# Optimization experiments

Measured on AMD Instinct MI355X. Metric: run time of the kernel, lower is better.

## Reference

```python
import jax, jax.numpy as jnp
import numpy as np

B, D, E, H = 4, 128, 512, 512

def setup_inputs() -> dict:
    key = jax.random.key(0)
    k1, k2, k3, k4, k5 = jax.random.split(key, 5)
    s = 1.0 / np.sqrt(H)
    return {
        "x_decoder": jax.random.normal(k1, (B, D, H), dtype=jnp.float32),
        "x_encoder": jax.random.normal(k2, (B, E, H), dtype=jnp.float32),
        "mask": jnp.zeros((B, E), dtype=bool),
        "W1": jax.random.uniform(k3, (H, H), jnp.float32, -s, s),  # nn.Linear weight (out,in)
        "W2": jax.random.uniform(k4, (H, H), jnp.float32, -s, s),
        "v": jax.random.uniform(k5, (H,), jnp.float32, -s, s),     # Linear(H,1) weight squeezed
    }

def reference(x_decoder, x_encoder, mask, W1, W2, v):
    # w1(x_encoder): (B,E,H); w2(x_decoder): (B,D,H)
    enc_t = jnp.einsum('beh,oh->beo', x_encoder, W1)
    dec_t = jnp.einsum('bdh,oh->bdo', x_decoder, W2)
    # additive attention: tanh over broadcast sum (B,D,E,H), reduce with v -> (B,D,E)
    prod = jnp.einsum('bdeh,h->bde', jnp.tanh(dec_t[:, :, None, :] + enc_t[:, None, :, :]), v)
    prod = jnp.where(mask[:, None, :], -jnp.inf, prod)
    return jax.nn.log_softmax(prod, axis=-1)
```

## Files before the change

### kernel.cpp

```cpp
#include <hip/hip_runtime.h>
#include <math.h>

#define BATCH 4
#define DDIM  128
#define EDIM  512
#define HDIM  512

#define TANH_SCALE 2.8853900817779268f

typedef short short8v __attribute__((ext_vector_type(8)));
typedef float f32x4   __attribute__((ext_vector_type(4)));
typedef float f32x2   __attribute__((ext_vector_type(2)));

#define EXP2F(x) __builtin_amdgcn_exp2f(x)
#define RCPF(x)  __builtin_amdgcn_rcpf(x)

static __device__ inline unsigned short f2bf(float f) {
    unsigned u = __float_as_uint(f);
    return (unsigned short)((u + 0x7FFFu + ((u >> 16) & 1u)) >> 16);
}
static __device__ inline unsigned pack_bf2(float f0, float f1) {
    unsigned u0 = __float_as_uint(f0), u1 = __float_as_uint(f1);
    u0 += 0x7FFFu + ((u0 >> 16) & 1u);
    u1 += 0x7FFFu + ((u1 >> 16) & 1u);
    return __builtin_amdgcn_perm(u1, u0, 0x07060302u);
}
static __device__ inline float bf2f(unsigned short h) {
    return __uint_as_float(((unsigned)h) << 16);
}

__global__ __launch_bounds__(256)
void gemm_both(const float* __restrict__ xdec, const float* __restrict__ W2,
               const float* __restrict__ xenc, const float* __restrict__ W1,
               unsigned short* __restrict__ P, unsigned short* __restrict__ Q) {
    __shared__ unsigned short As[2][64][40];
    __shared__ unsigned short Bs[2][64][40];

    const int id = blockIdx.x;
    const float *Ab, *Bb;
    unsigned short* Cb;
    int m0, n0;
    if (id < 64) {
        int b = id >> 4, r = id & 15;
        m0 = (r >> 3) * 64; n0 = (r & 7) * 64;
        Ab = xdec + (long)b * DDIM * HDIM;
        Bb = W2;
        Cb = P + (long)b * DDIM * HDIM;
    } else {
        int t2 = id - 64;
        int b = t2 >> 6, r = t2 & 63;
        m0 = (r >> 3) * 64; n0 = (r & 7) * 64;
        Ab = W1;
        Bb = xenc + (long)b * EDIM * HDIM;
        Cb = Q + (long)b * HDIM * EDIM;
    }

    const int t    = threadIdx.x;
    const int srow = t >> 2;
    const int skq  = (t & 3) << 3;

    const int wid = t >> 6, wm = wid >> 1, wn = wid & 1;
    const int l   = t & 63, lr = l & 15, c16 = l >> 4;

    f32x4 acc[2][2] = {};

    const float* ap = Ab + (long)(m0 + srow) * HDIM + skq;
    const float* bp = Bb + (long)(n0 + srow) * HDIM + skq;

    float4 a0 = *(const float4*)ap, a1 = *(const float4*)(ap + 4);
    float4 b0 = *(const float4*)bp, b1 = *(const float4*)(bp + 4);

    int cur = 0;
    for (int k0 = 0; k0 < HDIM; k0 += 32) {
        uint4 apk, bpk;
        apk.x = pack_bf2(a0.x, a0.y); apk.y = pack_bf2(a0.z, a0.w);
        apk.z = pack_bf2(a1.x, a1.y); apk.w = pack_bf2(a1.z, a1.w);
        bpk.x = pack_bf2(b0.x, b0.y); bpk.y = pack_bf2(b0.z, b0.w);
        bpk.z = pack_bf2(b1.x, b1.y); bpk.w = pack_bf2(b1.z, b1.w);
        *(uint4*)&As[cur][srow][skq] = apk;
        *(uint4*)&Bs[cur][srow][skq] = bpk;

        if (k0 + 32 < HDIM) {
            ap += 32; bp += 32;
            a0 = *(const float4*)ap; a1 = *(const float4*)(ap + 4);
            b0 = *(const float4*)bp; b1 = *(const float4*)(bp + 4);
        }

        asm volatile("s_waitcnt lgkmcnt(0)" ::: "memory");
        __builtin_amdgcn_s_barrier();
        __builtin_amdgcn_sched_barrier(0);

        short8v af[2], bf[2];
        #pragma unroll
        for (int fm = 0; fm < 2; ++fm)
            af[fm] = *(const short8v*)&As[cur][wm * 32 + fm * 16 + lr][c16 * 8];
        #pragma unroll
        for (int fn = 0; fn < 2; ++fn)
            bf[fn] = *(const short8v*)&Bs[cur][wn * 32 + fn * 16 + lr][c16 * 8];
        #pragma unroll
        for (int fm = 0; fm < 2; ++fm)
            #pragma unroll
            for (int fn = 0; fn < 2; ++fn)
                acc[fm][fn] = __builtin_amdgcn_mfma_f32_16x16x32_bf16(
                    af[fm], bf[fn], acc[fm][fn], 0, 0, 0);
        cur ^= 1;
    }

    const int crow = c16 << 2;
    #pragma unroll
    for (int fm = 0; fm < 2; ++fm)
        #pragma unroll
        for (int fn = 0; fn < 2; ++fn)
            #pragma unroll
            for (int r = 0; r < 4; ++r) {
                int rr = m0 + wm * 32 + fm * 16 + crow + r;
                int cc = n0 + wn * 32 + fn * 16 + lr;
                Cb[(long)rr * 512 + cc] = f2bf(EXP2F(TANH_SCALE * acc[fm][fn][r]));
            }
}

__global__ __launch_bounds__(1024)
void attn_lsm(const unsigned short* __restrict__ P,
              const unsigned short* __restrict__ Q,
              const unsigned char* __restrict__ mask,
              const float* __restrict__ vw,
              float* __restrict__ out) {
    const int g    = blockIdx.x;
    const int xcd  = g & 7;
    const int b    = xcd & 3;
    const int dp   = (g >> 3) + ((xcd >> 2) << 5);
    const int pair = b * 64 + dp;
    const int bd0  = pair * 2;
    const int t    = threadIdx.x;
    const int eq   = t & 127;
    const int hg   = t >> 7;

    __shared__ f32x2 combo2[256][3];
    __shared__ float lds[8][128][9];
    __shared__ float red[16];

    if (t < 256) {
        int h = t * 2;
        f32x2 p0, p1, vv;
        p0.x = bf2f(P[bd0 * HDIM + h]);       p0.y = bf2f(P[bd0 * HDIM + h + 1]);
        p1.x = bf2f(P[(bd0 + 1) * HDIM + h]); p1.y = bf2f(P[(bd0 + 1) * HDIM + h + 1]);
        vv.x = -2.0f * vw[h];                 vv.y = -2.0f * vw[h + 1];
        combo2[t][0] = p0; combo2[t][1] = p1; combo2[t][2] = vv;
    }
    __syncthreads();

    const unsigned short* qb = Q + b * HDIM * EDIM + (hg * 64) * EDIM + eq * 4;
    float a00 = 0.f, a01 = 0.f, a02 = 0.f, a03 = 0.f;
    float a10 = 0.f, a11 = 0.f, a12 = 0.f, a13 = 0.f;
    f32x2 ones; ones.x = 1.0f; ones.y = 1.0f;

#define PAIR_SET(Pp, q0p, q1p, VV, accA, accB)                                  \
    {                                                                           \
        f32x2 xp, yp, den, tt, num;                                             \
        asm("v_pk_fma_f32 %0, %1, %2, %3 op_sel_hi:[0,1,1]"                     \
            : "=v"(xp) : "v"(Pp), "v"(q0p), "v"(ones));                         \
        asm("v_pk_fma_f32 %0, %1, %2, %3 op_sel:[1,0,0] op_sel_hi:[1,1,1]"      \
            : "=v"(yp) : "v"(Pp), "v"(q1p), "v"(ones));                         \
        asm("v_pk_mul_f32 %0, %1, %2" : "=v"(den) : "v"(xp), "v"(yp));          \
        asm("v_pk_mul_f32 %0, %1, %2 op_sel:[1,0] op_sel_hi:[1,1]"              \
            : "=v"(tt) : "v"(VV), "v"(xp));                                     \
        asm("v_pk_fma_f32 %0, %1, %2, %3 op_sel_hi:[0,1,1]"                     \
            : "=v"(num) : "v"(VV), "v"(yp), "v"(tt));                           \
        accA = fmaf(num.x, RCPF(den.x), accA);                                  \
        accB = fmaf(num.y, RCPF(den.y), accB);                                  \
    }

    #pragma unroll 4
    for (int ii = 0; ii < 32; ++ii) {
        uint2 qv0 = *(const uint2*)(qb + (size_t)(2 * ii) * EDIM);
        uint2 qv1 = *(const uint2*)(qb + (size_t)(2 * ii + 1) * EDIM);
        f32x2 P0 = combo2[hg * 32 + ii][0];
        f32x2 P1 = combo2[hg * 32 + ii][1];
        f32x2 VV = combo2[hg * 32 + ii][2];
        f32x2 qA0, qB0, qA1, qB1;
        qA0.x = __uint_as_float(qv0.x << 16);
        qA0.y = __uint_as_float(qv0.x & 0xffff0000u);
        qB0.x = __uint_as_float(qv0.y << 16);
        qB0.y = __uint_as_float(qv0.y & 0xffff0000u);
        qA1.x = __uint_as_float(qv1.x << 16);
        qA1.y = __uint_as_float(qv1.x & 0xffff0000u);
        qB1.x = __uint_as_float(qv1.y << 16);
        qB1.y = __uint_as_float(qv1.y & 0xffff0000u);

        PAIR_SET(P0, qA0, qA1, VV, a00, a01);
        PAIR_SET(P0, qB0, qB1, VV, a02, a03);
        PAIR_SET(P1, qA0, qA1, VV, a10, a11);
        PAIR_SET(P1, qB0, qB1, VV, a12, a13);
    }
#undef PAIR_SET

    float* myl = &lds[hg][eq][0];
    myl[0] = a00; myl[1] = a01; myl[2] = a02; myl[3] = a03;
    myl[4] = a10; myl[5] = a11; myl[6] = a12; myl[7] = a13;
    __syncthreads();

    const int d = t >> 9, e = t & 511;
    const int j = d * 4 + (e & 3), eqi = e >> 2;
    float acc = ((lds[0][eqi][j] + lds[1][eqi][j]) +
                 (lds[2][eqi][j] + lds[3][eqi][j])) +
                ((lds[4][eqi][j] + lds[5][eqi][j]) +
                 (lds[6][eqi][j] + lds[7][eqi][j]));

    const bool mk = mask[b * EDIM + e];
    float val = mk ? -INFINITY : acc;

    const int wv = t >> 6, lid = t & 63, dg8 = d * 8;

    float m = val;
    #pragma unroll
    for (int o = 32; o >= 1; o >>= 1) m = fmaxf(m, __shfl_xor(m, o));
    if (lid == 0) red[wv] = m;
    __syncthreads();
    m = red[dg8];
    #pragma unroll
    for (int i = 1; i < 8; ++i) m = fmaxf(m, red[dg8 + i]);
    __syncthreads();

    float s = __expf(val - m);
    #pragma unroll
    for (int o = 32; o >= 1; o >>= 1) s += __shfl_xor(s, o);
    if (lid == 0) red[wv] = s;
    __syncthreads();
    float tot = 0.f;
    #pragma unroll
    for (int i = 0; i < 8; ++i) tot += red[dg8 + i];

    out[(long)(bd0 + d) * EDIM + e] = val - m - __logf(tot);
}

extern "C" void kernel_launch(void* const* d_in, const int* in_sizes, int n_in,
                              void* d_out, int out_size, void* d_ws, size_t ws_size,
                              hipStream_t stream) {
    const float*         xdec = (const float*)d_in[0];
    const float*         xenc = (const float*)d_in[1];
    const unsigned char* mask = (const unsigned char*)d_in[2];
    const float*         W1   = (const float*)d_in[3];
    const float*         W2   = (const float*)d_in[4];
    const float*         vw   = (const float*)d_in[5];
    float*               out  = (float*)d_out;

    unsigned short* P = (unsigned short*)d_ws;
    unsigned short* Q = P + 262144;

    gemm_both<<<320, 256, 0, stream>>>(xdec, W2, xenc, W1, P, Q);
    attn_lsm<<<256, 1024, 0, stream>>>(P, Q, mask, vw, out);
}
```

Measured before the change: 30.61 us.

## Combine four h-terms per reciprocal and widen Q loads to 16 bytes

The attention kernel now merges two pairs of rational tanh terms over a common denominator, so each group of four h values needs one reciprocal per output lane instead of two. Threads are remapped to cover 8 encoder columns and 32 h rows using uint4 loads of Q, with 16 h-groups instead of 8. The cross-thread reduction therefore adds 16 partials from a new LDS layout. It trades reciprocals and load instructions for extra packed multiplies, more LDS traffic, and a wider product of four denominators that risks overflow or precision loss.

```diff
diff --git a/kernel.cpp b/kernel.cpp
--- a/kernel.cpp
+++ b/kernel.cpp
@@ -28,6 +28,8 @@
 static __device__ inline float bf2f(unsigned short h) {
     return __uint_as_float(((unsigned)h) << 16);
 }
+static __device__ inline float blo(unsigned u) { return __uint_as_float(u << 16); }
+static __device__ inline float bhi(unsigned u) { return __uint_as_float(u & 0xffff0000u); }
 
 __global__ __launch_bounds__(256)
 void gemm_both(const float* __restrict__ xdec, const float* __restrict__ W2,
@@ -132,11 +134,11 @@
     const int pair = b * 64 + dp;
     const int bd0  = pair * 2;
     const int t    = threadIdx.x;
-    const int eq   = t & 127;
-    const int hg   = t >> 7;
+    const int eq   = t & 63;
+    const int hg   = t >> 6;
 
     __shared__ f32x2 combo2[256][3];
-    __shared__ float lds[8][128][9];
+    __shared__ float lds_red[16][16][64];
     __shared__ float red[16];
 
     if (t < 256) {
@@ -149,62 +151,97 @@
     }
     __syncthreads();
 
-    const unsigned short* qb = Q + b * HDIM * EDIM + (hg * 64) * EDIM + eq * 4;
-    float a00 = 0.f, a01 = 0.f, a02 = 0.f, a03 = 0.f;
-    float a10 = 0.f, a11 = 0.f, a12 = 0.f, a13 = 0.f;
+    const unsigned short* qb = Q + b * HDIM * EDIM + (hg * 32) * EDIM + eq * 8;
+    f32x2 acc2[2][4] = {};
     f32x2 ones; ones.x = 1.0f; ones.y = 1.0f;
 
-#define PAIR_SET(Pp, q0p, q1p, VV, accA, accB)                                  \
+#define QUAD(P01, P23, VV01, VV23, q0, q1, q2, q3, accp)                        \
     {                                                                           \
-        f32x2 xp, yp, den, tt, num;                                             \
-        asm("v_pk_fma_f32 %0, %1, %2, %3 op_sel_hi:[0,1,1]"                     \
-            : "=v"(xp) : "v"(Pp), "v"(q0p), "v"(ones));                         \
+        f32x2 x0, x1, x2, x3, d1, d2, t1, n1, t2, n2, nn, n, den;               \
+        asm("v_pk_fma_f32 %0, %1, %2, %3 op_sel_hi:[0,1,1]"                     \
+            : "=v"(x0) : "v"(P01), "v"(q0), "v"(ones));                         \
         asm("v_pk_fma_f32 %0, %1, %2, %3 op_sel:[1,0,0] op_sel_hi:[1,1,1]"      \
-            : "=v"(yp) : "v"(Pp), "v"(q1p), "v"(ones));                         \
-        asm("v_pk_mul_f32 %0, %1, %2" : "=v"(den) : "v"(xp), "v"(yp));          \
+            : "=v"(x1) : "v"(P01), "v"(q1), "v"(ones));                         \
+        asm("v_pk_fma_f32 %0, %1, %2, %3 op_sel_hi:[0,1,1]"                     \
+            : "=v"(x2) : "v"(P23), "v"(q2), "v"(ones));                         \
+        asm("v_pk_fma_f32 %0, %1, %2, %3 op_sel:[1,0,0] op_sel_hi:[1,1,1]"      \
+            : "=v"(x3) : "v"(P23), "v"(q3), "v"(ones));                         \
+        asm("v_pk_mul_f32 %0, %1, %2" : "=v"(d1) : "v"(x0), "v"(x1));           \
+        asm("v_pk_mul_f32 %0, %1, %2" : "=v"(d2) : "v"(x2), "v"(x3));           \
         asm("v_pk_mul_f32 %0, %1, %2 op_sel:[1,0] op_sel_hi:[1,1]"              \
-            : "=v"(tt) : "v"(VV), "v"(xp));                                     \
-        asm("v_pk_fma_f32 %0, %1, %2, %3 op_sel_hi:[0,1,1]"                     \
-            : "=v"(num) : "v"(VV), "v"(yp), "v"(tt));                           \
-        accA = fmaf(num.x, RCPF(den.x), accA);                                  \
-        accB = fmaf(num.y, RCPF(den.y), accB);                                  \
-    }
-
-    #pragma unroll 4
-    for (int ii = 0; ii < 32; ++ii) {
-        uint2 qv0 = *(const uint2*)(qb + (size_t)(2 * ii) * EDIM);
-        uint2 qv1 = *(const uint2*)(qb + (size_t)(2 * ii + 1) * EDIM);
-        f32x2 P0 = combo2[hg * 32 + ii][0];
-        f32x2 P1 = combo2[hg * 32 + ii][1];
-        f32x2 VV = combo2[hg * 32 + ii][2];
-        f32x2 qA0, qB0, qA1, qB1;
-        qA0.x = __uint_as_float(qv0.x << 16);
-        qA0.y = __uint_as_float(qv0.x & 0xffff0000u);
-        qB0.x = __uint_as_float(qv0.y << 16);
-        qB0.y = __uint_as_float(qv0.y & 0xffff0000u);
-        qA1.x = __uint_as_float(qv1.x << 16);
-        qA1.y = __uint_as_float(qv1.x & 0xffff0000u);
-        qB1.x = __uint_as_float(qv1.y << 16);
-        qB1.y = __uint_as_float(qv1.y & 0xffff0000u);
-
-        PAIR_SET(P0, qA0, qA1, VV, a00, a01);
-        PAIR_SET(P0, qB0, qB1, VV, a02, a03);
-        PAIR_SET(P1, qA0, qA1, VV, a10, a11);
-        PAIR_SET(P1, qB0, qB1, VV, a12, a13);
-    }
-#undef PAIR_SET
-
-    float* myl = &lds[hg][eq][0];
-    myl[0] = a00; myl[1] = a01; myl[2] = a02; myl[3] = a03;
-    myl[4] = a10; myl[5] = a11; myl[6] = a12; myl[7] = a13;
+            : "=v"(t1) : "v"(VV01), "v"(x0));                                   \
+        asm("v_pk_fma_f32 %0, %1, %2, %3 op_sel_hi:[0,1,1]"                     \
+            : "=v"(n1) : "v"(VV01), "v"(x1), "v"(t1));                          \
+        asm("v_pk_mul_f32 %0, %1, %2 op_sel:[1,0] op_sel_hi:[1,1]"              \
+            : "=v"(t2) : "v"(VV23), "v"(x2));                                   \
+        asm("v_pk_fma_f32 %0, %1, %2, %3 op_sel_hi:[0,1,1]"                     \
+            : "=v"(n2) : "v"(VV23), "v"(x3), "v"(t2));                          \
+        asm("v_pk_mul_f32 %0, %1, %2" : "=v"(nn) : "v"(n1), "v"(d2));           \
+        asm("v_pk_fma_f32 %0, %1, %2, %3" : "=v"(n) : "v"(n2), "v"(d1), "v"(nn));\
+        asm("v_pk_mul_f32 %0, %1, %2" : "=v"(den) : "v"(d1), "v"(d2));          \
+        accp.x = fmaf(n.x, RCPF(den.x), accp.x);                                \
+        accp.y = fmaf(n.y, RCPF(den.y), accp.y);                                \
+    }
+
+    #pragma unroll 2
+    for (int k = 0; k < 8; ++k) {
+        uint4 r0 = *(const uint4*)(qb + (size_t)(k * 4 + 0) * EDIM);
+        uint4 r1 = *(const uint4*)(qb + (size_t)(k * 4 + 1) * EDIM);
+        uint4 r2 = *(const uint4*)(qb + (size_t)(k * 4 + 2) * EDIM);
+        uint4 r3 = *(const uint4*)(qb + (size_t)(k * 4 + 3) * EDIM);
+
+        f32x2 qr[4][4];
+        qr[0][0].x = blo(r0.x); qr[0][0].y = bhi(r0.x);
+        qr[0][1].x = blo(r0.y); qr[0][1].y = bhi(r0.y);
+        qr[0][2].x = blo(r0.z); qr[0][2].y = bhi(r0.z);
+        qr[0][3].x = blo(r0.w); qr[0][3].y = bhi(r0.w);
+        qr[1][0].x = blo(r1.x); qr[1][0].y = bhi(r1.x);
+        qr[1][1].x = blo(r1.y); qr[1][1].y = bhi(r1.y);
+        qr[1][2].x = blo(r1.z); qr[1][2].y = bhi(r1.z);
+        qr[1][3].x = blo(r1.w); qr[1][3].y = bhi(r1.w);
+        qr[2][0].x = blo(r2.x); qr[2][0].y = bhi(r2.x);
+        qr[2][1].x = blo(r2.y); qr[2][1].y = bhi(r2.y);
+        qr[2][2].x = blo(r2.z); qr[2][2].y = bhi(r2.z);
+        qr[2][3].x = blo(r2.w); qr[2][3].y = bhi(r2.w);
+        qr[3][0].x = blo(r3.x); qr[3][0].y = bhi(r3.x);
+        qr[3][1].x = blo(r3.y); qr[3][1].y = bhi(r3.y);
+        qr[3][2].x = blo(r3.z); qr[3][2].y = bhi(r3.z);
+        qr[3][3].x = blo(r3.w); qr[3][3].y = bhi(r3.w);
+
+        const int hp0 = hg * 16 + k * 2;
+        f32x2 P01d0 = combo2[hp0][0],     P23d0 = combo2[hp0 + 1][0];
+        f32x2 P01d1 = combo2[hp0][1],     P23d1 = combo2[hp0 + 1][1];
+        f32x2 VV01  = combo2[hp0][2],     VV23  = combo2[hp0 + 1][2];
+
+        #pragma unroll
+        for (int ep = 0; ep < 4; ++ep) {
+            QUAD(P01d0, P23d0, VV01, VV23,
+                 qr[0][ep], qr[1][ep], qr[2][ep], qr[3][ep], acc2[0][ep]);
+            QUAD(P01d1, P23d1, VV01, VV23,
+                 qr[0][ep], qr[1][ep], qr[2][ep], qr[3][ep], acc2[1][ep]);
+        }
+    }
+#undef QUAD
+
+    #pragma unroll
+    for (int d = 0; d < 2; ++d)
+        #pragma unroll
+        for (int ep = 0; ep < 4; ++ep) {
+            lds_red[d * 8 + ep * 2 + 0][hg][eq] = acc2[d][ep].x;
+            lds_red[d * 8 + ep * 2 + 1][hg][eq] = acc2[d][ep].y;
+        }
     __syncthreads();
 
     const int d = t >> 9, e = t & 511;
-    const int j = d * 4 + (e & 3), eqi = e >> 2;
-    float acc = ((lds[0][eqi][j] + lds[1][eqi][j]) +
-                 (lds[2][eqi][j] + lds[3][eqi][j])) +
-                ((lds[4][eqi][j] + lds[5][eqi][j]) +
-                 (lds[6][eqi][j] + lds[7][eqi][j]));
+    const int ei = e >> 3, j = d * 8 + (e & 7);
+    float acc = (((lds_red[j][0][ei]  + lds_red[j][1][ei]) +
+                  (lds_red[j][2][ei]  + lds_red[j][3][ei])) +
+                 ((lds_red[j][4][ei]  + lds_red[j][5][ei]) +
+                  (lds_red[j][6][ei]  + lds_red[j][7][ei]))) +
+                (((lds_red[j][8][ei]  + lds_red[j][9][ei]) +
+                  (lds_red[j][10][ei] + lds_red[j][11][ei])) +
+                 ((lds_red[j][12][ei] + lds_red[j][13][ei]) +
+                  (lds_red[j][14][ei] + lds_red[j][15][ei])));
 
     const bool mk = mask[b * EDIM + e];
     float val = mk ? -INFINITY : acc;
```

After: 31.28 us. 2.2% more time.
